# Optimization experiments

Hardware: AMD Instinct MI355X
Metric: run time of the kernel (lower is better)

The kernel has to match this reference:

```python
import jax, jax.numpy as jnp
import numpy as np

ALPHA = 1.0
INF = 1e4  # larger than any possible distance in a 256x256 image


def _row_dist_to_zero(x):
    """1D distance along last axis to nearest zero pixel. x: [..., W] (0/1)."""
    W = x.shape[-1]
    idx = jnp.arange(W, dtype=jnp.float32)
    is0 = x == 0
    # nearest zero at-or-before each position
    last0 = jax.lax.cummax(jnp.where(is0, idx, -1.0), axis=x.ndim - 1)
    fwd = jnp.where(last0 >= 0, idx - last0, INF)
    # nearest zero at-or-after each position (suffix max of -idx)
    neg_next0 = jax.lax.cummax(jnp.where(is0, -idx, -INF), axis=x.ndim - 1, reverse=True)
    bwd = jnp.where(neg_next0 > -INF, (-neg_next0) - idx, INF)
    return jnp.minimum(fwd, bwd)


def _edt_2d(target):
    """Exact Euclidean distance transform per [B,C] map: distance from nonzero
    pixels to nearest zero pixel (matches scipy.ndimage.distance_transform_edt)."""
    B, C, H, W = target.shape
    g = _row_dist_to_zero(target)            # [B,C,H,W] distance along width
    g2 = g * g
    i = jnp.arange(H, dtype=jnp.float32)
    dk2 = (i[:, None] - i[None, :]) ** 2     # [H(out), H(k)]
    # dt2[b,c,i,w] = min_k g2[b,c,k,w] + (i-k)^2
    d2 = jnp.min(g2[:, :, None, :, :] + dk2[None, None, :, :, None], axis=3)
    return jnp.sqrt(d2)


def _distance_map(target):
    dist = _edt_2d(target)
    dmax = jnp.max(dist, axis=(-2, -1), keepdims=True)
    return dist / (dmax + 1e-7)


def setup_inputs() -> dict:
    key = jax.random.key(0)
    k1, k2 = jax.random.split(key)
    pred = jax.random.normal(k1, (8, 1, 256, 256), dtype=jnp.float32)
    target = jax.random.randint(k2, (8, 1, 256, 256), 0, 2).astype(jnp.float32)
    return {"pred": pred, "target": target}


def reference(pred, target):
    dist_map = _distance_map(target)
    weight_map = 1.0 + ALPHA * dist_map
    # numerically stable BCE with logits, reduction='none'
    bce = jnp.maximum(pred, 0.0) - pred * target + jnp.log1p(jnp.exp(-jnp.abs(pred)))
    return jnp.mean(weight_map * bce)
```

## Files before the change

### kernel.cpp

```cpp
#include <hip/hip_runtime.h>
#include <math.h>

#define BATCH 8
#define H 256
#define W 256
#define NPIX (BATCH * H * W)
#define NBLK2 1024

__device__ __forceinline__ float bce_logits(float p, float t) {
    return fmaxf(p, 0.0f) - p * t + log1pf(expf(-fabsf(p)));
}

__global__ void __launch_bounds__(256) row_edt(const float* __restrict__ target,
                                               unsigned short* __restrict__ d16) {
    __shared__ unsigned long long mlds[4][4];
    const int tid = threadIdx.x;
    const int v = tid >> 6, l = tid & 63;
    const float* imgr = target + (size_t)blockIdx.x * 4 * W;

    #pragma unroll
    for (int j = 0; j < 4; ++j) {
        float t = imgr[j * W + tid];
        unsigned long long m = __ballot(t == 0.0f);
        if (l == 0) mlds[j][v] = m;
    }
    __syncthreads();

    const int p = tid;
    #pragma unroll
    for (int j = 0; j < 4; ++j) {
        unsigned long long mw[4] = {mlds[j][0], mlds[j][1], mlds[j][2], mlds[j][3]};
        int best = 1 << 20;
        #pragma unroll
        for (int w = 0; w < 4; ++w) {
            const int rel = p - (w << 6);
            const unsigned long long m = mw[w];
            unsigned long long mlo = (rel < 0)  ? 0ull
                                   : (rel >= 63) ? m : (m & ((2ull << rel) - 1ull));
            unsigned long long mhi = (rel <= 0) ? m
                                   : (rel > 63)  ? 0ull : (m & (~0ull << rel));
            if (mlo) best = min(best, rel - (63 - __builtin_clzll(mlo)));
            if (mhi) best = min(best, __builtin_ctzll(mhi) - rel);
        }
        d16[(size_t)blockIdx.x * 4 * W + j * W + tid] =
            (best > 255) ? (unsigned short)10000 : (unsigned short)best;
    }
}

__global__ void __launch_bounds__(256) envelope_bce(
        const unsigned short* __restrict__ d16, const float* __restrict__ pred,
        float* __restrict__ pmx, float* __restrict__ psb, float* __restrict__ psdb) {
    __shared__ float red[3][4];
    const int tid = threadIdx.x;
    const int wv = tid >> 6, l = tid & 63;
    const int b  = blockIdx.x >> 7;
    const int cs = (blockIdx.x >> 5) & 3;
    const int rs = blockIdx.x & 31;
    const int c  = (cs << 6) + l;
    const int i0 = (rs << 3) + (wv << 1);

    const size_t po = ((size_t)(b * H + i0)) * W + c;
    float p0 = pred[po], p1 = pred[po + W];

    const unsigned short* gcol = d16 + (size_t)b * H * W + c;

    float acc0 = 3.0e38f, acc1 = 3.0e38f;
    const int P = 10;
    #pragma unroll
    for (int s = 0; s < P; ++s) {
        const int kd = i0 + 1 - s;
        const int ku = i0 + 2 + s;
        float dd = (float)gcol[(size_t)max(kd, 0) * W];
        float du = (float)gcol[(size_t)min(ku, 255) * W];
        float gd = dd * dd, gu = du * du;
        if (kd < 0)   gd = 3.0e38f;
        if (ku > 255) gu = 3.0e38f;
        const float ed0 = (float)(s - 1), ed1 = (float)s;
        const float eu0 = (float)(s + 2), eu1 = (float)(s + 1);
        acc0 = fminf(acc0, fminf(fmaf(ed0, ed0, gd), fmaf(eu0, eu0, gu)));
        acc1 = fminf(acc1, fminf(fmaf(ed1, ed1, gd), fmaf(eu1, eu1, gu)));
    }

    int kd = i0 + 1 - P, ku = i0 + 2 + P;
    float fd0 = (float)(i0 - kd);
    float fu0 = (float)(ku - i0);
    for (;;) {
        float maxacc = fmaxf(acc0, acc1);
        float dn = (float)(i0 - kd);
        float up = (float)(ku - (i0 + 1));
        bool alive = (kd >= 0 && dn * dn <= maxacc) || (ku <= 255 && up * up <= maxacc);
        if (!__any(alive)) break;
        if (kd >= 0) {
            float dv = (float)gcol[(size_t)kd * W];
            float g = dv * dv;
            acc0 = fminf(acc0, fmaf(fd0, fd0, g));
            float fd1 = fd0 + 1.0f;
            acc1 = fminf(acc1, fmaf(fd1, fd1, g));
        }
        if (ku <= 255) {
            float dv = (float)gcol[(size_t)ku * W];
            float g = dv * dv;
            float fu1 = fu0 - 1.0f;
            acc0 = fminf(acc0, fmaf(fu0, fu0, g));
            acc1 = fminf(acc1, fmaf(fu1, fu1, g));
        }
        --kd; ++ku; fd0 += 1.0f; fu0 += 1.0f;
    }

    float t0 = (acc0 == 0.0f) ? 0.0f : 1.0f;
    float t1 = (acc1 == 0.0f) ? 0.0f : 1.0f;
    float mx = fmaxf(acc0, acc1);
    float b0 = bce_logits(p0, t0), b1 = bce_logits(p1, t1);
    float sb  = b0 + b1;
    float sdb = sqrtf(acc0) * b0 + sqrtf(acc1) * b1;

    #pragma unroll
    for (int o = 32; o > 0; o >>= 1) {
        mx  = fmaxf(mx, __shfl_down(mx, o, 64));
        sb  += __shfl_down(sb, o, 64);
        sdb += __shfl_down(sdb, o, 64);
    }
    if (l == 0) { red[0][wv] = mx; red[1][wv] = sb; red[2][wv] = sdb; }
    __syncthreads();
    if (tid == 0) {
        pmx [blockIdx.x] = fmaxf(fmaxf(red[0][0], red[0][1]), fmaxf(red[0][2], red[0][3]));
        psb [blockIdx.x] = (red[1][0] + red[1][1]) + (red[1][2] + red[1][3]);
        psdb[blockIdx.x] = (red[2][0] + red[2][1]) + (red[2][2] + red[2][3]);
    }
}

__global__ void final_reduce(const float* __restrict__ pmx, const float* __restrict__ psb,
                             const float* __restrict__ psdb, float* __restrict__ out) {
    const int tid = threadIdx.x;
    const int img = tid >> 5, j = tid & 31;
    float mx = 0.0f, sb = 0.0f, sdb = 0.0f;
    #pragma unroll
    for (int q = 0; q < 4; ++q) {
        const int e = (img << 7) + j + (q << 5);
        mx  = fmaxf(mx, pmx[e]);
        sb  += psb[e];
        sdb += psdb[e];
    }
    #pragma unroll
    for (int o = 16; o > 0; o >>= 1) {
        mx  = fmaxf(mx, __shfl_down(mx, o, 32));
        sb  += __shfl_down(sb, o, 32);
        sdb += __shfl_down(sdb, o, 32);
    }
    __shared__ float cimg[8], simg[8];
    if (j == 0) {
        cimg[img] = sdb / (sqrtf(mx) + 1e-7f);
        simg[img] = sb;
    }
    __syncthreads();
    if (tid == 0) {
        float tot = 0.0f;
        #pragma unroll
        for (int i = 0; i < 8; ++i) tot += simg[i] + cimg[i];
        out[0] = tot * (1.0f / (float)NPIX);
    }
}

extern "C" void kernel_launch(void* const* d_in, const int* in_sizes, int n_in,
                              void* d_out, int out_size, void* d_ws, size_t ws_size,
                              hipStream_t stream) {
    const float* pred   = (const float*)d_in[0];
    const float* target = (const float*)d_in[1];

    unsigned short* d16 = (unsigned short*)d_ws;
    float* pmx  = (float*)((char*)d_ws + (size_t)NPIX * sizeof(unsigned short));
    float* psb  = pmx + NBLK2;
    float* psdb = psb + NBLK2;

    row_edt<<<BATCH * 64, 256, 0, stream>>>(target, d16);
    envelope_bce<<<NBLK2, 256, 0, stream>>>(d16, pred, pmx, psb, psdb);
    final_reduce<<<1, 256, 0, stream>>>(pmx, psb, psdb, (float*)d_out);
}
```

Measured before the change: 65.84 us.

## Fuse row EDT and column envelope into one strip-per-block kernel

Merges the row distance kernel and the column envelope/BCE kernel into a single 1024-thread kernel. Each block owns an 8-column strip of one image and recomputes the zero-pixel ballot masks for the whole image into LDS. It then keeps the row distances for its strip in an LDS tile, so the 16-bit distance map no longer round-trips through global memory and one kernel launch disappears. The cost is that every block rereads the full target image (a 32x redundant read served from cache), pred loads are only 8 floats wide per row, and the grid shrinks to 256 large blocks.

New measurement: 80.96 us. 23.0% more time.

```diff
diff --git a/kernel.cpp b/kernel.cpp
--- a/kernel.cpp
+++ b/kernel.cpp
@@ -5,35 +5,57 @@
 #define H 256
 #define W 256
 #define NPIX (BATCH * H * W)
-#define NBLK2 1024
+#define COLS 8
+#define STRIPS (W / COLS)
+#define NBLKA (BATCH * STRIPS)
 
 __device__ __forceinline__ float bce_logits(float p, float t) {
     return fmaxf(p, 0.0f) - p * t + log1pf(expf(-fabsf(p)));
 }
 
-__global__ void __launch_bounds__(256) row_edt(const float* __restrict__ target,
-                                               unsigned short* __restrict__ d16) {
-    __shared__ unsigned long long mlds[4][4];
+__global__ void __launch_bounds__(1024) fused_edt_bce(
+        const float* __restrict__ target, const float* __restrict__ pred,
+        float* __restrict__ pmx, float* __restrict__ psb, float* __restrict__ psdb) {
+    __shared__ unsigned long long mlds[4][H];
+    __shared__ unsigned short dtile[H][COLS + 2];
+    __shared__ float red[3][16];
+
     const int tid = threadIdx.x;
-    const int v = tid >> 6, l = tid & 63;
-    const float* imgr = target + (size_t)blockIdx.x * 4 * W;
+    const int wv = tid >> 6, l = tid & 63;
+    const int b     = blockIdx.x >> 5;
+    const int strip = blockIdx.x & 31;
+    const int c0 = strip << 3;
 
-    #pragma unroll
-    for (int j = 0; j < 4; ++j) {
-        float t = imgr[j * W + tid];
-        unsigned long long m = __ballot(t == 0.0f);
-        if (l == 0) mlds[j][v] = m;
+    const int cc = tid & 7;
+    const int tg = tid >> 3;
+    const int i0 = tg << 1;
+    const int gc = c0 + cc;
+
+    const size_t po = ((size_t)(b * H + i0)) * W + gc;
+    const float p0 = pred[po], p1 = pred[po + W];
+
+    const float* img = target + (size_t)b * (H * W);
+    #pragma unroll 16
+    for (int i = 0; i < 64; ++i) {
+        const int q   = (wv << 6) + i;
+        const int row = q >> 2, ch = q & 3;
+        const float t = img[row * W + (ch << 6) + l];
+        const unsigned long long m = __ballot(t == 0.0f);
+        if (l == 0) mlds[ch][row] = m;
     }
     __syncthreads();
 
-    const int p = tid;
     #pragma unroll
-    for (int j = 0; j < 4; ++j) {
-        unsigned long long mw[4] = {mlds[j][0], mlds[j][1], mlds[j][2], mlds[j][3]};
+    for (int r2 = 0; r2 < 2; ++r2) {
+        const int p   = tid + (r2 << 10);
+        const int row = p >> 3;
+        const int pc  = c0 + (p & 7);
+        const unsigned long long mw[4] =
+            {mlds[0][row], mlds[1][row], mlds[2][row], mlds[3][row]};
         int best = 1 << 20;
         #pragma unroll
         for (int w = 0; w < 4; ++w) {
-            const int rel = p - (w << 6);
+            const int rel = pc - (w << 6);
             const unsigned long long m = mw[w];
             unsigned long long mlo = (rel < 0)  ? 0ull
                                    : (rel >= 63) ? m : (m & ((2ull << rel) - 1ull));
@@ -42,27 +64,10 @@
             if (mlo) best = min(best, rel - (63 - __builtin_clzll(mlo)));
             if (mhi) best = min(best, __builtin_ctzll(mhi) - rel);
         }
-        d16[(size_t)blockIdx.x * 4 * W + j * W + tid] =
-            (best > 255) ? (unsigned short)10000 : (unsigned short)best;
+        dtile[row][p & 7] = (best > 255) ? (unsigned short)10000
+                                         : (unsigned short)best;
     }
-}
-
-__global__ void __launch_bounds__(256) envelope_bce(
-        const unsigned short* __restrict__ d16, const float* __restrict__ pred,
-        float* __restrict__ pmx, float* __restrict__ psb, float* __restrict__ psdb) {
-    __shared__ float red[3][4];
-    const int tid = threadIdx.x;
-    const int wv = tid >> 6, l = tid & 63;
-    const int b  = blockIdx.x >> 7;
-    const int cs = (blockIdx.x >> 5) & 3;
-    const int rs = blockIdx.x & 31;
-    const int c  = (cs << 6) + l;
-    const int i0 = (rs << 3) + (wv << 1);
-
-    const size_t po = ((size_t)(b * H + i0)) * W + c;
-    float p0 = pred[po], p1 = pred[po + W];
-
-    const unsigned short* gcol = d16 + (size_t)b * H * W + c;
+    __syncthreads();
 
     float acc0 = 3.0e38f, acc1 = 3.0e38f;
     const int P = 10;
@@ -70,8 +75,8 @@
     for (int s = 0; s < P; ++s) {
         const int kd = i0 + 1 - s;
         const int ku = i0 + 2 + s;
-        float dd = (float)gcol[(size_t)max(kd, 0) * W];
-        float du = (float)gcol[(size_t)min(ku, 255) * W];
+        float dd = (float)dtile[max(kd, 0)][cc];
+        float du = (float)dtile[min(ku, 255)][cc];
         float gd = dd * dd, gu = du * du;
         if (kd < 0)   gd = 3.0e38f;
         if (ku > 255) gu = 3.0e38f;
@@ -80,7 +85,6 @@
         acc0 = fminf(acc0, fminf(fmaf(ed0, ed0, gd), fmaf(eu0, eu0, gu)));
         acc1 = fminf(acc1, fminf(fmaf(ed1, ed1, gd), fmaf(eu1, eu1, gu)));
     }
-
     int kd = i0 + 1 - P, ku = i0 + 2 + P;
     float fd0 = (float)(i0 - kd);
     float fu0 = (float)(ku - i0);
@@ -91,14 +95,14 @@
         bool alive = (kd >= 0 && dn * dn <= maxacc) || (ku <= 255 && up * up <= maxacc);
         if (!__any(alive)) break;
         if (kd >= 0) {
-            float dv = (float)gcol[(size_t)kd * W];
+            float dv = (float)dtile[kd][cc];
             float g = dv * dv;
             acc0 = fminf(acc0, fmaf(fd0, fd0, g));
             float fd1 = fd0 + 1.0f;
             acc1 = fminf(acc1, fmaf(fd1, fd1, g));
         }
         if (ku <= 255) {
-            float dv = (float)gcol[(size_t)ku * W];
+            float dv = (float)dtile[ku][cc];
             float g = dv * dv;
             float fu1 = fu0 - 1.0f;
             acc0 = fminf(acc0, fmaf(fu0, fu0, g));
@@ -123,9 +127,16 @@
     if (l == 0) { red[0][wv] = mx; red[1][wv] = sb; red[2][wv] = sdb; }
     __syncthreads();
     if (tid == 0) {
-        pmx [blockIdx.x] = fmaxf(fmaxf(red[0][0], red[0][1]), fmaxf(red[0][2], red[0][3]));
-        psb [blockIdx.x] = (red[1][0] + red[1][1]) + (red[1][2] + red[1][3]);
-        psdb[blockIdx.x] = (red[2][0] + red[2][1]) + (red[2][2] + red[2][3]);
+        float m2 = red[0][0], s2 = red[1][0], d2 = red[2][0];
+        #pragma unroll
+        for (int k = 1; k < 16; ++k) {
+            m2 = fmaxf(m2, red[0][k]);
+            s2 += red[1][k];
+            d2 += red[2][k];
+        }
+        pmx [blockIdx.x] = m2;
+        psb [blockIdx.x] = s2;
+        psdb[blockIdx.x] = d2;
     }
 }
 
@@ -133,14 +144,8 @@
                              const float* __restrict__ psdb, float* __restrict__ out) {
     const int tid = threadIdx.x;
     const int img = tid >> 5, j = tid & 31;
-    float mx = 0.0f, sb = 0.0f, sdb = 0.0f;
-    #pragma unroll
-    for (int q = 0; q < 4; ++q) {
-        const int e = (img << 7) + j + (q << 5);
-        mx  = fmaxf(mx, pmx[e]);
-        sb  += psb[e];
-        sdb += psdb[e];
-    }
+    const int e = (img << 5) + j;
+    float mx = pmx[e], sb = psb[e], sdb = psdb[e];
     #pragma unroll
     for (int o = 16; o > 0; o >>= 1) {
         mx  = fmaxf(mx, __shfl_down(mx, o, 32));
@@ -167,12 +172,10 @@
     const float* pred   = (const float*)d_in[0];
     const float* target = (const float*)d_in[1];
 
-    unsigned short* d16 = (unsigned short*)d_ws;
-    float* pmx  = (float*)((char*)d_ws + (size_t)NPIX * sizeof(unsigned short));
-    float* psb  = pmx + NBLK2;
-    float* psdb = psb + NBLK2;
+    float* pmx  = (float*)d_ws;
+    float* psb  = pmx + NBLKA;
+    float* psdb = psb + NBLKA;
 
-    row_edt<<<BATCH * 64, 256, 0, stream>>>(target, d16);
-    envelope_bce<<<NBLK2, 256, 0, stream>>>(d16, pred, pmx, psb, psdb);
+    fused_edt_bce<<<NBLKA, 1024, 0, stream>>>(target, pred, pmx, psb, psdb);
     final_reduce<<<1, 256, 0, stream>>>(pmx, psb, psdb, (float*)d_out);
 }
```

## Fuse row EDT into envelope kernel with shared-memory halo tile

Applied to the files above, without the earlier changes.

Removes the separate row_edt kernel and the global d16 intermediate. Each block ballots the target rows in a 32-row window (8 output rows plus a 12-row halo on each side) into shared-memory masks, computes row distances for its 64 columns into an LDS tile, and runs the column envelope from that tile. If any thread's search leaves the window, the block falls back to loading masks for the whole image and computing row distances on the fly. This saves a kernel launch and the global round trip, but recomputes row distances redundantly across the four column-slice blocks and adds the fallback path.

Measured after the change: 77.02 us. 17.0% more time.

```diff
diff --git a/kernel.cpp b/kernel.cpp
--- a/kernel.cpp
+++ b/kernel.cpp
@@ -11,46 +11,29 @@
     return fmaxf(p, 0.0f) - p * t + log1pf(expf(-fabsf(p)));
 }
 
-__global__ void __launch_bounds__(256) row_edt(const float* __restrict__ target,
-                                               unsigned short* __restrict__ d16) {
-    __shared__ unsigned long long mlds[4][4];
-    const int tid = threadIdx.x;
-    const int v = tid >> 6, l = tid & 63;
-    const float* imgr = target + (size_t)blockIdx.x * 4 * W;
-
-    #pragma unroll
-    for (int j = 0; j < 4; ++j) {
-        float t = imgr[j * W + tid];
-        unsigned long long m = __ballot(t == 0.0f);
-        if (l == 0) mlds[j][v] = m;
-    }
-    __syncthreads();
-
-    const int p = tid;
-    #pragma unroll
-    for (int j = 0; j < 4; ++j) {
-        unsigned long long mw[4] = {mlds[j][0], mlds[j][1], mlds[j][2], mlds[j][3]};
-        int best = 1 << 20;
-        #pragma unroll
-        for (int w = 0; w < 4; ++w) {
-            const int rel = p - (w << 6);
-            const unsigned long long m = mw[w];
-            unsigned long long mlo = (rel < 0)  ? 0ull
-                                   : (rel >= 63) ? m : (m & ((2ull << rel) - 1ull));
-            unsigned long long mhi = (rel <= 0) ? m
-                                   : (rel > 63)  ? 0ull : (m & (~0ull << rel));
-            if (mlo) best = min(best, rel - (63 - __builtin_clzll(mlo)));
-            if (mhi) best = min(best, __builtin_ctzll(mhi) - rel);
-        }
-        d16[(size_t)blockIdx.x * 4 * W + j * W + tid] =
-            (best > 255) ? (unsigned short)10000 : (unsigned short)best;
-    }
-}
-
-__global__ void __launch_bounds__(256) envelope_bce(
-        const unsigned short* __restrict__ d16, const float* __restrict__ pred,
+__device__ __forceinline__ int rowdist_scan(const unsigned long long mw[4], int p) {
+    int best = 1 << 20;
+    #pragma unroll
+    for (int w = 0; w < 4; ++w) {
+        const int rel = p - (w << 6);
+        const unsigned long long m = mw[w];
+        unsigned long long mlo = (rel < 0)  ? 0ull
+                               : (rel >= 63) ? m : (m & ((2ull << rel) - 1ull));
+        unsigned long long mhi = (rel <= 0) ? m
+                               : (rel > 63)  ? 0ull : (m & (~0ull << rel));
+        if (mlo) best = min(best, rel - (63 - __builtin_clzll(mlo)));
+        if (mhi) best = min(best, __builtin_ctzll(mhi) - rel);
+    }
+    return best;
+}
+
+__global__ void __launch_bounds__(256) fused_edt_bce(
+        const float* __restrict__ target, const float* __restrict__ pred,
         float* __restrict__ pmx, float* __restrict__ psb, float* __restrict__ psdb) {
+    __shared__ unsigned long long msk[256][4];
+    __shared__ unsigned short dtile[32][64];
     __shared__ float red[3][4];
+
     const int tid = threadIdx.x;
     const int wv = tid >> 6, l = tid & 63;
     const int b  = blockIdx.x >> 7;
@@ -59,10 +42,33 @@
     const int c  = (cs << 6) + l;
     const int i0 = (rs << 3) + (wv << 1);
 
+    const int win0 = (rs << 3) - 12;
+    const int wlo = max(win0, 0), whi = min(win0 + 31, 255);
+
     const size_t po = ((size_t)(b * H + i0)) * W + c;
     float p0 = pred[po], p1 = pred[po + W];
 
-    const unsigned short* gcol = d16 + (size_t)b * H * W + c;
+    const float* img = target + (size_t)b * (H * W);
+
+    #pragma unroll 8
+    for (int i = 0; i < 32; ++i) {
+        const int q = (wv << 5) + i;
+        const int j = q >> 2, ch = q & 3;
+        const int row = min(max(win0 + j, 0), 255);
+        const float t = img[row * W + (ch << 6) + l];
+        const unsigned long long m = __ballot(t == 0.0f);
+        if (l == 0) msk[j][ch] = m;
+    }
+    __syncthreads();
+
+    #pragma unroll
+    for (int i = 0; i < 8; ++i) {
+        const int j = wv + (i << 2);
+        const unsigned long long mw[4] = {msk[j][0], msk[j][1], msk[j][2], msk[j][3]};
+        const int best = rowdist_scan(mw, c);
+        dtile[j][l] = (best > 255) ? (unsigned short)10000 : (unsigned short)best;
+    }
+    __syncthreads();
 
     float acc0 = 3.0e38f, acc1 = 3.0e38f;
     const int P = 10;
@@ -70,8 +76,9 @@
     for (int s = 0; s < P; ++s) {
         const int kd = i0 + 1 - s;
         const int ku = i0 + 2 + s;
-        float dd = (float)gcol[(size_t)max(kd, 0) * W];
-        float du = (float)gcol[(size_t)min(ku, 255) * W];
+        const int rd = max(kd, 0), ru = min(ku, 255);
+        float dd = (float)dtile[rd - win0][l];
+        float du = (float)dtile[ru - win0][l];
         float gd = dd * dd, gu = du * du;
         if (kd < 0)   gd = 3.0e38f;
         if (ku > 255) gu = 3.0e38f;
@@ -84,27 +91,68 @@
     int kd = i0 + 1 - P, ku = i0 + 2 + P;
     float fd0 = (float)(i0 - kd);
     float fu0 = (float)(ku - i0);
+    bool beyond = false;
     for (;;) {
         float maxacc = fmaxf(acc0, acc1);
         float dn = (float)(i0 - kd);
         float up = (float)(ku - (i0 + 1));
         bool alive = (kd >= 0 && dn * dn <= maxacc) || (ku <= 255 && up * up <= maxacc);
         if (!__any(alive)) break;
+        if ((kd >= 0 && kd < wlo) || (ku <= 255 && ku > whi)) { beyond = true; break; }
         if (kd >= 0) {
-            float dv = (float)gcol[(size_t)kd * W];
+            float dv = (float)dtile[kd - win0][l];
             float g = dv * dv;
             acc0 = fminf(acc0, fmaf(fd0, fd0, g));
             float fd1 = fd0 + 1.0f;
             acc1 = fminf(acc1, fmaf(fd1, fd1, g));
         }
         if (ku <= 255) {
-            float dv = (float)gcol[(size_t)ku * W];
+            float dv = (float)dtile[ku - win0][l];
             float g = dv * dv;
             float fu1 = fu0 - 1.0f;
             acc0 = fminf(acc0, fmaf(fu0, fu0, g));
             acc1 = fminf(acc1, fmaf(fu1, fu1, g));
         }
         --kd; ++ku; fd0 += 1.0f; fu0 += 1.0f;
+    }
+
+    const unsigned need = (unsigned)__syncthreads_count(beyond ? 1 : 0);
+    if (need) {
+        #pragma unroll 4
+        for (int i = 0; i < 256; ++i) {
+            const int q = (wv << 8) + i;
+            const int row = q >> 2, ch = q & 3;
+            const float t = img[row * W + (ch << 6) + l];
+            const unsigned long long m = __ballot(t == 0.0f);
+            if (l == 0) msk[row][ch] = m;
+        }
+        __syncthreads();
+        for (;;) {
+            float maxacc = fmaxf(acc0, acc1);
+            float dn = (float)(i0 - kd);
+            float up = (float)(ku - (i0 + 1));
+            bool alive = (kd >= 0 && dn * dn <= maxacc) || (ku <= 255 && up * up <= maxacc);
+            if (!__any(alive)) break;
+            if (kd >= 0) {
+                const unsigned long long mw[4] = {msk[kd][0], msk[kd][1], msk[kd][2], msk[kd][3]};
+                const int best = rowdist_scan(mw, c);
+                float dv = (best > 255) ? 10000.0f : (float)best;
+                float g = dv * dv;
+                acc0 = fminf(acc0, fmaf(fd0, fd0, g));
+                float fd1 = fd0 + 1.0f;
+                acc1 = fminf(acc1, fmaf(fd1, fd1, g));
+            }
+            if (ku <= 255) {
+                const unsigned long long mw[4] = {msk[ku][0], msk[ku][1], msk[ku][2], msk[ku][3]};
+                const int best = rowdist_scan(mw, c);
+                float dv = (best > 255) ? 10000.0f : (float)best;
+                float g = dv * dv;
+                float fu1 = fu0 - 1.0f;
+                acc0 = fminf(acc0, fmaf(fu0, fu0, g));
+                acc1 = fminf(acc1, fmaf(fu1, fu1, g));
+            }
+            --kd; ++ku; fd0 += 1.0f; fu0 += 1.0f;
+        }
     }
 
     float t0 = (acc0 == 0.0f) ? 0.0f : 1.0f;
@@ -167,12 +215,10 @@
     const float* pred   = (const float*)d_in[0];
     const float* target = (const float*)d_in[1];
 
-    unsigned short* d16 = (unsigned short*)d_ws;
-    float* pmx  = (float*)((char*)d_ws + (size_t)NPIX * sizeof(unsigned short));
+    float* pmx  = (float*)d_ws;
     float* psb  = pmx + NBLK2;
     float* psdb = psb + NBLK2;
 
-    row_edt<<<BATCH * 64, 256, 0, stream>>>(target, d16);
-    envelope_bce<<<NBLK2, 256, 0, stream>>>(d16, pred, pmx, psb, psdb);
+    fused_edt_bce<<<NBLK2, 256, 0, stream>>>(target, pred, pmx, psb, psdb);
     final_reduce<<<1, 256, 0, stream>>>(pmx, psb, psdb, (float*)d_out);
 }
```
